# Performance work log

Hardware: AMD Instinct MI355X
Metric: run time of the kernel (lower is better)

## Reference

```python
import jax, jax.numpy as jnp
import numpy as np

HIDDEN = 3072
HEADS = 32
HEAD_DIM = HIDDEN // HEADS  # 96


def setup_inputs() -> dict:
    key = jax.random.key(0)
    k1, k2, k3, k4 = jax.random.split(key, 4)
    B, S = 2, 2048
    x = jax.random.normal(k1, (B, S, HIDDEN), dtype=jnp.float32)
    # qkv_proj: Linear(hidden, 3*hidden, bias=False); torch weight is [out,in]
    w_qkv = jax.random.normal(k2, (3 * HIDDEN, HIDDEN), dtype=jnp.float32) * (HIDDEN ** -0.5)
    # o_proj: Linear(hidden, hidden) with bias
    w_o = jax.random.normal(k3, (HIDDEN, HIDDEN), dtype=jnp.float32) * (HIDDEN ** -0.5)
    b_o = jax.random.normal(k4, (HIDDEN,), dtype=jnp.float32) * 0.01
    return {"x": x, "w_qkv": w_qkv, "w_o": w_o, "b_o": b_o}


def reference(x, w_qkv, w_o, b_o):
    B, S, _ = x.shape
    qkv = jnp.einsum('bsh,oh->bso', x, w_qkv)  # [B,S,3*HIDDEN]
    q, k, v = jnp.split(qkv, 3, axis=-1)
    # [B,S,HIDDEN] -> [B,H,S,D]
    def split_heads(t):
        return t.reshape(B, S, HEADS, HEAD_DIM).transpose(0, 2, 1, 3)
    q, k, v = split_heads(q), split_heads(k), split_heads(v)
    scores = jnp.einsum('bhqd,bhkd->bhqk', q, k) / jnp.sqrt(jnp.float32(HEAD_DIM))
    attn = jax.nn.softmax(scores, axis=-1)
    out = jnp.einsum('bhqk,bhkd->bhqd', attn, v)  # [B,H,S,D]
    out = out.transpose(0, 2, 1, 3).reshape(B, S, HIDDEN)
    return jnp.einsum('bsh,oh->bso', out, w_o) + b_o
```

## Files before the change

### kernel.cpp

```cpp
#include <hip/hip_runtime.h>
#include <math.h>


typedef unsigned int u32;
typedef unsigned short u16;
typedef __attribute__((ext_vector_type(8))) short bf16x8;
typedef __attribute__((ext_vector_type(4))) float f32x4;
typedef __attribute__((ext_vector_type(16))) float f32x16;

#define MFMA(a, b, c) __builtin_amdgcn_mfma_f32_16x16x32_bf16((a), (b), (c), 0, 0, 0)
#define MFMA32(a, b, c) __builtin_amdgcn_mfma_f32_32x32x16_bf16((a), (b), (c), 0, 0, 0)

#define GLDS16(g, l) __builtin_amdgcn_global_load_lds( \
    (const __attribute__((address_space(1))) u32*)(g), \
    (__attribute__((address_space(3))) u32*)(l), 16, 0, 0)

__device__ __forceinline__ u16 f2bf(float f) {
  u32 u = __builtin_bit_cast(u32, f);
  return (u16)((u + 0x7fffu + ((u >> 16) & 1u)) >> 16);
}
__device__ __forceinline__ float bf2f(u16 h) {
  u32 u = ((u32)h) << 16;
  return __builtin_bit_cast(float, u);
}
__device__ __forceinline__ void split2(float f, u16& h, u16& l) {
  h = f2bf(f);
  l = f2bf(f - bf2f(h));
}
__device__ __forceinline__ bf16x8 ld16(const u16* p) {
  return *reinterpret_cast<const bf16x8*>(p);
}

__global__ void split_kernel(const float* __restrict__ src, u16* __restrict__ dst,
                             long n) {
  long i = ((long)blockIdx.x * 256 + threadIdx.x) * 8;
  if (i >= n) return;
  const float4 v0 = *reinterpret_cast<const float4*>(src + i);
  const float4 v1 = *reinterpret_cast<const float4*>(src + i + 4);
  const u32 i32 = (u32)i;
  const u32 row = i32 / 3072u;
  const u32 col = i32 - row * 3072u;
  const long base = (long)row * 6144 + (col >> 5) * 64 + (col & 31);
  bf16x8 hv, lv;
  u16 h, l;
  split2(v0.x, h, l); hv[0] = (short)h; lv[0] = (short)l;
  split2(v0.y, h, l); hv[1] = (short)h; lv[1] = (short)l;
  split2(v0.z, h, l); hv[2] = (short)h; lv[2] = (short)l;
  split2(v0.w, h, l); hv[3] = (short)h; lv[3] = (short)l;
  split2(v1.x, h, l); hv[4] = (short)h; lv[4] = (short)l;
  split2(v1.y, h, l); hv[5] = (short)h; lv[5] = (short)l;
  split2(v1.z, h, l); hv[6] = (short)h; lv[6] = (short)l;
  split2(v1.w, h, l); hv[7] = (short)h; lv[7] = (short)l;
  *reinterpret_cast<bf16x8*>(dst + base) = hv;
  *reinterpret_cast<bf16x8*>(dst + base + 32) = lv;
}

template <int MODE>
__global__ __launch_bounds__(256, 2) void gemm32(
    const u16* __restrict__ A2, const u16* __restrict__ B2,
    int M, int N, u16* __restrict__ C2, u16* __restrict__ Kp,
    u16* __restrict__ Vp, float* __restrict__ Cf, const float* __restrict__ bias) {
  constexpr int NT = 96;
  __shared__ u16 shm[2 * 128 * 64 + 2 * 192 * 64];
  u16* const uA = shm;
  u16* const uB = shm + 2 * 128 * 64;
  const int tid = threadIdx.x;
  const int lane = tid & 63;
  const int w = tid >> 6;
  const int wm = w >> 1, wn = w & 1;
  const int l31 = lane & 31;
  const int l5 = lane >> 5;

  const int mt = M >> 7;
  const int nwg = gridDim.x;
  const int bid = blockIdx.x;
  const int wg = (bid & 7) * (nwg >> 3) + (bid >> 3);
  const int bm = wg % mt, bn = wg / mt;

  const int srow = lane >> 3;
  const int sgc = ((lane & 7) ^ srow ^ w) * 8;

  auto stA = [&](int buf, int kt, int j) {
    const int r = j * 32 + w * 8 + srow;
    GLDS16(A2 + (long)(bm * 128 + r) * 6144 + kt * 64 + sgc,
           &uA[buf * 8192 + (j * 32 + w * 8) * 64]);
  };
  auto stB = [&](int buf, int kt, int j) {
    const int r = j * 32 + w * 8 + srow;
    GLDS16(B2 + (long)(bn * 192 + r) * 6144 + kt * 64 + sgc,
           &uB[buf * 12288 + (j * 32 + w * 8) * 64]);
  };

  f32x16 acc[2][3];
#pragma unroll
  for (int m = 0; m < 2; ++m)
#pragma unroll
    for (int n = 0; n < 3; ++n)
#pragma unroll
      for (int j = 0; j < 16; ++j) acc[m][n][j] = 0.f;

  stA(0, 0, 0); stA(0, 0, 1); stA(0, 0, 2); stA(0, 0, 3);
  stB(0, 0, 0); stB(0, 0, 1); stB(0, 0, 2);
  stB(0, 0, 3); stB(0, 0, 4); stB(0, 0, 5);
  __syncthreads();

  const int aRow0 = wm * 64 + l31;
  const int bRow0 = wn * 96 + l31;
  const int rk = (lane & 7) ^ ((lane >> 3) & 3);

#define CSLOT(KS, PL) ((((KS)*2 + l5 + (PL)*4) ^ rk) * 8)
#define RD_PH(KS)                                                          \
  _Pragma("unroll") for (int n = 0; n < 3; ++n) {                          \
    const int off = (bRow0 + n * 32) * 64;                                 \
    b[n][0] = ld16(&LB[off + CSLOT(KS, 0)]);                               \
    b[n][1] = ld16(&LB[off + CSLOT(KS, 1)]);                               \
  }                                                                        \
  _Pragma("unroll") for (int m = 0; m < 2; ++m) {                          \
    const int off = (aRow0 + m * 32) * 64;                                 \
    a[m][0] = ld16(&LA[off + CSLOT(KS, 0)]);                               \
    a[m][1] = ld16(&LA[off + CSLOT(KS, 1)]);                               \
  }
#define DO_MFMA3()                                                         \
  __builtin_amdgcn_s_setprio(1);                                           \
  _Pragma("unroll") for (int m = 0; m < 2; ++m)                            \
  _Pragma("unroll") for (int n = 0; n < 3; ++n) {                          \
    acc[m][n] = MFMA32(a[m][0], b[n][0], acc[m][n]);                       \
    acc[m][n] = MFMA32(a[m][0], b[n][1], acc[m][n]);                       \
    acc[m][n] = MFMA32(a[m][1], b[n][0], acc[m][n]);                       \
  }                                                                        \
  __builtin_amdgcn_s_setprio(0);
#define PH_SYNC()                                                          \
  __builtin_amdgcn_s_barrier();                                            \
  asm volatile("s_waitcnt lgkmcnt(0)" ::: "memory");                       \
  __builtin_amdgcn_sched_barrier(0);

  for (int t = 0; t < NT; ++t) {
    const int cur = t & 1;
    const int nxt = cur ^ 1;
    const u16* LA = &uA[cur * 8192];
    const u16* LB = &uB[cur * 12288];
    bf16x8 a[2][2], b[3][2];
    RD_PH(0);
    if (t + 1 < NT) {
      stA(nxt, t + 1, 0); stA(nxt, t + 1, 1);
      stA(nxt, t + 1, 2); stA(nxt, t + 1, 3);
      stB(nxt, t + 1, 0); stB(nxt, t + 1, 1); stB(nxt, t + 1, 2);
      stB(nxt, t + 1, 3); stB(nxt, t + 1, 4); stB(nxt, t + 1, 5);
    }
    PH_SYNC();
    DO_MFMA3();
    __builtin_amdgcn_s_barrier();
    RD_PH(1);
    PH_SYNC();
    DO_MFMA3();
    asm volatile("s_waitcnt vmcnt(0)" ::: "memory");
    __builtin_amdgcn_s_barrier();
  }
#undef CSLOT
#undef RD_PH
#undef DO_MFMA3
#undef PH_SYNC

  if (MODE == 1 || (MODE == 2 && bn < 16)) {
#pragma unroll
    for (int mf = 0; mf < 2; ++mf)
#pragma unroll
      for (int nf = 0; nf < 3; ++nf) {
        const int col = bn * 192 + wn * 96 + nf * 32 + l31;
#pragma unroll
        for (int reg = 0; reg < 16; ++reg) {
          const int rif = (reg & 3) + 8 * (reg >> 2) + 4 * l5;
          const long row = (long)bm * 128 + wm * 64 + mf * 32 + rif;
          const float v = acc[mf][nf][reg];
          if (MODE == 1) {
            Cf[row * N + col] = v + bias[col];
          } else {
            const long idx = row * 6144 + (col >> 5) * 64 + (col & 31);
            u16 h, l;
            split2(v, h, l);
            C2[idx] = h;
            C2[idx + 32] = l;
          }
        }
      }
  } else if (MODE == 2) {
    const bool isV = (bn >= 32);
    const int hd0 = (bn - (isV ? 32 : 16)) * 2;
    const int b = (bm * 128) >> 11;
    const int s_loc = (bm * 128) & 2047;
    u16* const P = shm;
    u16* const dst = isV ? Vp : Kp;
#pragma unroll
    for (int hf = 0; hf < 2; ++hf) {
      __syncthreads();
      if (wm == hf) {
#pragma unroll
        for (int mf = 0; mf < 2; ++mf)
#pragma unroll
          for (int nf = 0; nf < 3; ++nf)
#pragma unroll
            for (int reg = 0; reg < 16; ++reg) {
              const int rif = (reg & 3) + 8 * (reg >> 2) + 4 * l5;
              const int row_l = mf * 32 + rif;
              const int col_l = wn * 96 + nf * 32 + l31;
              u16 h, l;
              split2(acc[mf][nf][reg], h, l);
              P[row_l * 200 + col_l] = h;
              P[(64 + row_l) * 200 + col_l] = l;
            }
      }
      __syncthreads();
      const int lr = lane & 15, lg = lane >> 4;
      if (!isV) {
#pragma unroll
        for (int i = 0; i < 12; ++i) {
          const int ri = w * 12 + i;
          const int pl = ri & 1;
          const int kbi = (ri >> 1) & 3;
          const int c = (ri >> 3) % 3;
          const int hh = ri / 24;
          const bf16x8 v =
              ld16(&P[(pl * 64 + kbi * 16 + lr) * 200 + hh * 96 + c * 32 + lg * 8]);
          const int hl = b * 32 + hd0 + hh;
          const int kbg = ((s_loc + hf * 64) >> 4) + kbi;
          const long rec3 = ((long)hl * 128 + kbg) * 3 + c;
          *reinterpret_cast<bf16x8*>(dst + (rec3 * 2 + pl) * 512 + lane * 8) = v;
        }
      } else {
#pragma unroll
        for (int i = 0; i < 12; ++i) {
          const int ri = w * 12 + i;
          const int pl = ri & 1;
          const int kq = (ri >> 1) & 1;
          const int n = (ri >> 2) % 6;
          const int hh = ri / 24;
          bf16x8 v;
#pragma unroll
          for (int e = 0; e < 8; ++e)
            v[e] = (short)P[(pl * 64 + kq * 32 + lg * 8 + e) * 200 + hh * 96 + n * 16 + lr];
          const int hl = b * 32 + hd0 + hh;
          const int kqg = ((s_loc + hf * 64) >> 5) + kq;
          const long rec = (((long)hl * 6 + n) * 64 + kqg) * 2 + pl;
          *reinterpret_cast<bf16x8*>(dst + rec * 512 + lane * 8) = v;
        }
      }
    }
  }
}

__global__ __launch_bounds__(256, 2) void attn_kernel(
    const u16* __restrict__ Q2,
    const u16* __restrict__ Kp, const u16* __restrict__ Vp,
    u16* __restrict__ AO2) {
  __shared__ u16 kv[2][24 * 512];
  __shared__ u16 pb[4][2][2][512];
  const int lane = threadIdx.x & 63;
  const int wv = threadIdx.x >> 6;
  const int lr = lane & 15, lg = lane >> 4;

  const int nwg = gridDim.x;
  const int bid = blockIdx.x;
  const int wg = (bid & 7) * (nwg >> 3) + (bid >> 3);
  const int hl = wg >> 4;
  const int qblk = wg & 15;
  const int b = hl >> 5;
  const int q0 = qblk * 128 + wv * 32;

  bf16x8 qh[2][3], ql[2][3];
#pragma unroll
  for (int f = 0; f < 2; ++f) {
    const long qofs =
        ((long)(b * 2048 + q0 + f * 16 + lr)) * 6144 + ((hl & 31) * 3) * 64 + lg * 8;
#pragma unroll
    for (int c = 0; c < 3; ++c) {
      qh[f][c] = ld16(Q2 + qofs + c * 64);
      ql[f][c] = ld16(Q2 + qofs + c * 64 + 32);
    }
  }

  f32x4 o_acc[2][6];
#pragma unroll
  for (int f = 0; f < 2; ++f)
#pragma unroll
    for (int n = 0; n < 6; ++n)
#pragma unroll
      for (int j = 0; j < 4; ++j) o_acc[f][n][j] = 0.f;
  float lsum[2][4] = {{0.f, 0.f, 0.f, 0.f}, {0.f, 0.f, 0.f, 0.f}};

  const float scale = 0.10206207261596577f;

  auto stage = [&](int nb, int it) {
    const long kbase = ((long)hl * 768 + (long)it * 12) * 512;
    const long vbase = ((long)hl * 768 + (long)it * 2) * 512;
#pragma unroll
    for (int j = 0; j < 6; ++j) {
      const int r = wv * 6 + j;
      const u16* src;
      if (r < 12) {
        const int tt = r / 6, rc = r % 6;
        src = Kp + kbase + ((long)(tt * 6 + rc)) * 512 + lane * 8;
      } else {
        const int r2 = r - 12;
        src = Vp + vbase + ((long)((r2 >> 1) * 128 + (r2 & 1))) * 512 + lane * 8;
      }
      GLDS16(src, &kv[nb][r * 512]);
    }
  };

  stage(0, 0);
  __syncthreads();

  for (int it = 0; it < 64; ++it) {
    const int nb = it & 1;
    if (it < 63) stage(nb ^ 1, it + 1);
    const u16* L = kv[nb];

    bf16x8 kh0[3], kl0[3], kh1[3], kl1[3];
#pragma unroll
    for (int c = 0; c < 3; ++c) {
      kh0[c] = ld16(L + (c * 2 + 0) * 512 + lane * 8);
      kl0[c] = ld16(L + (c * 2 + 1) * 512 + lane * 8);
      kh1[c] = ld16(L + (6 + c * 2 + 0) * 512 + lane * 8);
      kl1[c] = ld16(L + (6 + c * 2 + 1) * 512 + lane * 8);
    }

    bf16x8 pah[2], pal[2];
#pragma unroll
    for (int f = 0; f < 2; ++f) {
      f32x4 s0, s1;
#pragma unroll
      for (int j = 0; j < 4; ++j) { s0[j] = 0.f; s1[j] = 0.f; }
#pragma unroll
      for (int c = 0; c < 3; ++c) {
        s0 = MFMA(qh[f][c], kh0[c], s0);
        s1 = MFMA(qh[f][c], kh1[c], s1);
        s0 = MFMA(qh[f][c], kl0[c], s0);
        s1 = MFMA(qh[f][c], kl1[c], s1);
        s0 = MFMA(ql[f][c], kh0[c], s0);
        s1 = MFMA(ql[f][c], kh1[c], s1);
      }
      u16* pbh = pb[wv][f][0];
      u16* pbl = pb[wv][f][1];
#pragma unroll
      for (int j = 0; j < 4; ++j) {
        const float p0 = __expf(fmaf(s0[j], scale, -12.f));
        const float p1 = __expf(fmaf(s1[j], scale, -12.f));
        lsum[f][j] += p0 + p1;
        const int r = lg * 4 + j;
        const int key = j ^ lg;
        u16 h, l;
        split2(p0, h, l);
        const int a0 = r * 32 + ((((lr >> 3) ^ key) & 3) << 3) + (lr & 7);
        pbh[a0] = h;
        pbl[a0] = l;
        split2(p1, h, l);
        const int a1 = r * 32 + ((((2 + (lr >> 3)) ^ key) & 3) << 3) + (lr & 7);
        pbh[a1] = h;
        pbl[a1] = l;
      }
      const int rkey = (lr & 3) ^ (lr >> 2);
      const int ra = lr * 32 + (((lg ^ rkey) & 3) << 3);
      pah[f] = ld16(&pbh[ra]);
      pal[f] = ld16(&pbl[ra]);
    }

#pragma unroll
    for (int n = 0; n < 6; ++n) {
      const bf16x8 vh = ld16(L + (12 + n * 2 + 0) * 512 + lane * 8);
      const bf16x8 vl = ld16(L + (12 + n * 2 + 1) * 512 + lane * 8);
#pragma unroll
      for (int f = 0; f < 2; ++f) {
        o_acc[f][n] = MFMA(pah[f], vh, o_acc[f][n]);
        o_acc[f][n] = MFMA(pah[f], vl, o_acc[f][n]);
        o_acc[f][n] = MFMA(pal[f], vh, o_acc[f][n]);
      }
    }
    __syncthreads();
  }

#pragma unroll
  for (int f = 0; f < 2; ++f) {
    float inv[4];
#pragma unroll
    for (int j = 0; j < 4; ++j) {
      float rs = lsum[f][j];
#pragma unroll
      for (int mk = 1; mk < 16; mk <<= 1) rs += __shfl_xor(rs, mk);
      inv[j] = 1.f / rs;
    }
#pragma unroll
    for (int n = 0; n < 6; ++n)
#pragma unroll
      for (int j = 0; j < 4; ++j) {
        const long row = (long)(b * 2048 + q0 + f * 16 + lg * 4 + j);
        const long idx =
            row * 6144 + ((hl & 31) * 3 + (n >> 1)) * 64 + (n & 1) * 16 + lr;
        u16 h, l;
        split2(o_acc[f][n][j] * inv[j], h, l);
        AO2[idx] = h;
        AO2[idx + 32] = l;
      }
  }
}

extern "C" void kernel_launch(void* const* d_in, const int* in_sizes, int n_in,
                              void* d_out, int out_size, void* d_ws, size_t ws_size,
                              hipStream_t stream) {
  const float* x = (const float*)d_in[0];
  const float* wqkv = (const float*)d_in[1];
  const float* wo = (const float*)d_in[2];
  const float* bo = (const float*)d_in[3];
  float* out = (float*)d_out;
  char* ws = (char*)d_ws;

  const size_t E_X = (size_t)4096 * 3072;
  const size_t E_WQ = (size_t)9216 * 3072;
  const size_t E_WO = (size_t)3072 * 3072;

  u16* X2 = (u16*)ws;
  char* W0 = ws + 4 * E_X;
  u16* W2 = (u16*)W0;
  u16* Q2 = (u16*)(W0 + 4 * E_WQ);
  u16* KP = Q2 + 2 * E_X;
  u16* VP = KP + 2 * E_X;
  u16* AO2 = (u16*)W0;
  u16* WO2 = (u16*)(W0 + 4 * E_X);

  const size_t need = 4 * (4 * E_X + E_WQ);
  if (ws_size < need) return;

  split_kernel<<<6144, 256, 0, stream>>>(x, X2, (long)E_X);
  split_kernel<<<13824, 256, 0, stream>>>(wqkv, W2, (long)E_WQ);
  gemm32<2><<<1536, 256, 0, stream>>>(X2, W2, 4096, 9216, Q2, KP, VP,
                                      nullptr, nullptr);
  split_kernel<<<4608, 256, 0, stream>>>(wo, WO2, (long)E_WO);
  attn_kernel<<<1024, 256, 0, stream>>>(Q2, KP, VP, AO2);
  gemm32<1><<<512, 256, 0, stream>>>(AO2, WO2, 4096, 3072, nullptr, nullptr,
                                     nullptr, out, bo);
}
```

Before: 1.166 ms.

## Stage only K tiles through LDS and load V directly from global

The attention loop now stages two K tiles per iteration into the LDS double buffer, halving the iteration count. V fragments are loaded straight from global memory into registers instead of going through LDS. This cuts LDS traffic and the number of barriers, but adds global-load latency on V that is not prefetched and raises register pressure. It also assumes the K/V layout produced upstream allows this indexing.

Result: slower. 1.242 ms (+6.5%).

```diff
diff --git a/kernel.cpp b/kernel.cpp
--- a/kernel.cpp
+++ b/kernel.cpp
@@ -290,90 +290,90 @@
   const float scale = 0.10206207261596577f;
 
   auto stage = [&](int nb, int it) {
-    const long kbase = ((long)hl * 768 + (long)it * 12) * 512;
-    const long vbase = ((long)hl * 768 + (long)it * 2) * 512;
+    const long base = ((long)hl * 768 + (long)it * 24) * 512;
 #pragma unroll
     for (int j = 0; j < 6; ++j) {
       const int r = wv * 6 + j;
-      const u16* src;
-      if (r < 12) {
-        const int tt = r / 6, rc = r % 6;
-        src = Kp + kbase + ((long)(tt * 6 + rc)) * 512 + lane * 8;
-      } else {
-        const int r2 = r - 12;
-        src = Vp + vbase + ((long)((r2 >> 1) * 128 + (r2 & 1))) * 512 + lane * 8;
-      }
-      GLDS16(src, &kv[nb][r * 512]);
+      GLDS16(Kp + base + (long)r * 512 + lane * 8, &kv[nb][r * 512]);
     }
   };
 
   stage(0, 0);
   __syncthreads();
 
-  for (int it = 0; it < 64; ++it) {
+  for (int it = 0; it < 32; ++it) {
     const int nb = it & 1;
-    if (it < 63) stage(nb ^ 1, it + 1);
-    const u16* L = kv[nb];
-
-    bf16x8 kh0[3], kl0[3], kh1[3], kl1[3];
-#pragma unroll
-    for (int c = 0; c < 3; ++c) {
-      kh0[c] = ld16(L + (c * 2 + 0) * 512 + lane * 8);
-      kl0[c] = ld16(L + (c * 2 + 1) * 512 + lane * 8);
-      kh1[c] = ld16(L + (6 + c * 2 + 0) * 512 + lane * 8);
-      kl1[c] = ld16(L + (6 + c * 2 + 1) * 512 + lane * 8);
-    }
-
-    bf16x8 pah[2], pal[2];
-#pragma unroll
-    for (int f = 0; f < 2; ++f) {
-      f32x4 s0, s1;
-#pragma unroll
-      for (int j = 0; j < 4; ++j) { s0[j] = 0.f; s1[j] = 0.f; }
+    if (it < 31) stage(nb ^ 1, it + 1);
+#pragma unroll
+    for (int h = 0; h < 2; ++h) {
+      const u16* L = kv[nb] + h * (12 * 512);
+
+      bf16x8 vh[6], vl[6];
+#pragma unroll
+      for (int n = 0; n < 6; ++n) {
+        const long ro =
+            ((((long)(hl * 6 + n)) * 64 + (it * 2 + h)) * 2) * 512 + lane * 8;
+        vh[n] = ld16(Vp + ro);
+        vl[n] = ld16(Vp + ro + 512);
+      }
+
+      bf16x8 kh0[3], kl0[3], kh1[3], kl1[3];
 #pragma unroll
       for (int c = 0; c < 3; ++c) {
-        s0 = MFMA(qh[f][c], kh0[c], s0);
-        s1 = MFMA(qh[f][c], kh1[c], s1);
-        s0 = MFMA(qh[f][c], kl0[c], s0);
-        s1 = MFMA(qh[f][c], kl1[c], s1);
-        s0 = MFMA(ql[f][c], kh0[c], s0);
-        s1 = MFMA(ql[f][c], kh1[c], s1);
-      }
-      u16* pbh = pb[wv][f][0];
-      u16* pbl = pb[wv][f][1];
-#pragma unroll
-      for (int j = 0; j < 4; ++j) {
-        const float p0 = __expf(fmaf(s0[j], scale, -12.f));
-        const float p1 = __expf(fmaf(s1[j], scale, -12.f));
-        lsum[f][j] += p0 + p1;
-        const int r = lg * 4 + j;
-        const int key = j ^ lg;
-        u16 h, l;
-        split2(p0, h, l);
-        const int a0 = r * 32 + ((((lr >> 3) ^ key) & 3) << 3) + (lr & 7);
-        pbh[a0] = h;
-        pbl[a0] = l;
-        split2(p1, h, l);
-        const int a1 = r * 32 + ((((2 + (lr >> 3)) ^ key) & 3) << 3) + (lr & 7);
-        pbh[a1] = h;
-        pbl[a1] = l;
-      }
-      const int rkey = (lr & 3) ^ (lr >> 2);
-      const int ra = lr * 32 + (((lg ^ rkey) & 3) << 3);
-      pah[f] = ld16(&pbh[ra]);
-      pal[f] = ld16(&pbl[ra]);
-    }
-
-#pragma unroll
-    for (int n = 0; n < 6; ++n) {
-      const bf16x8 vh = ld16(L + (12 + n * 2 + 0) * 512 + lane * 8);
-      const bf16x8 vl = ld16(L + (12 + n * 2 + 1) * 512 + lane * 8);
+        kh0[c] = ld16(L + (c * 2 + 0) * 512 + lane * 8);
+        kl0[c] = ld16(L + (c * 2 + 1) * 512 + lane * 8);
+        kh1[c] = ld16(L + (6 + c * 2 + 0) * 512 + lane * 8);
+        kl1[c] = ld16(L + (6 + c * 2 + 1) * 512 + lane * 8);
+      }
+
+      bf16x8 pah[2], pal[2];
 #pragma unroll
       for (int f = 0; f < 2; ++f) {
-        o_acc[f][n] = MFMA(pah[f], vh, o_acc[f][n]);
-        o_acc[f][n] = MFMA(pah[f], vl, o_acc[f][n]);
-        o_acc[f][n] = MFMA(pal[f], vh, o_acc[f][n]);
-      }
+        f32x4 s0, s1;
+#pragma unroll
+        for (int j = 0; j < 4; ++j) { s0[j] = 0.f; s1[j] = 0.f; }
+#pragma unroll
+        for (int c = 0; c < 3; ++c) {
+          s0 = MFMA(qh[f][c], kh0[c], s0);
+          s1 = MFMA(qh[f][c], kh1[c], s1);
+          s0 = MFMA(qh[f][c], kl0[c], s0);
+          s1 = MFMA(qh[f][c], kl1[c], s1);
+          s0 = MFMA(ql[f][c], kh0[c], s0);
+          s1 = MFMA(ql[f][c], kh1[c], s1);
+        }
+        u16* pbh = pb[wv][f][0];
+        u16* pbl = pb[wv][f][1];
+#pragma unroll
+        for (int j = 0; j < 4; ++j) {
+          const float p0 = __expf(fmaf(s0[j], scale, -12.f));
+          const float p1 = __expf(fmaf(s1[j], scale, -12.f));
+          lsum[f][j] += p0 + p1;
+          const int r = lg * 4 + j;
+          const int key = j ^ lg;
+          u16 hh, ll;
+          split2(p0, hh, ll);
+          const int a0 = r * 32 + ((((lr >> 3) ^ key) & 3) << 3) + (lr & 7);
+          pbh[a0] = hh;
+          pbl[a0] = ll;
+          split2(p1, hh, ll);
+          const int a1 = r * 32 + ((((2 + (lr >> 3)) ^ key) & 3) << 3) + (lr & 7);
+          pbh[a1] = hh;
+          pbl[a1] = ll;
+        }
+        const int rkey = (lr & 3) ^ (lr >> 2);
+        const int ra = lr * 32 + (((lg ^ rkey) & 3) << 3);
+        pah[f] = ld16(&pbh[ra]);
+        pal[f] = ld16(&pbl[ra]);
+      }
+
+#pragma unroll
+      for (int n = 0; n < 6; ++n)
+#pragma unroll
+        for (int f = 0; f < 2; ++f) {
+          o_acc[f][n] = MFMA(pah[f], vh[n], o_acc[f][n]);
+          o_acc[f][n] = MFMA(pah[f], vl[n], o_acc[f][n]);
+          o_acc[f][n] = MFMA(pal[f], vh[n], o_acc[f][n]);
+        }
     }
     __syncthreads();
   }
```
